# Optimization experiments

Measured on AMD Instinct MI355X. Metric: run time of the kernel, lower is better.

## Reference

```python
import jax, jax.numpy as jnp
import numpy as np

EMB = 1024
NHEAD = 16
HEAD_DIM = EMB // NHEAD  # 64
L = 2048
NEG = -1e30


def setup_inputs() -> dict:
    key = jax.random.key(0)
    ks = jax.random.split(key, 8)
    # xavier_uniform bound for square [EMB, EMB] matrices
    bound = float(np.sqrt(6.0 / (EMB + EMB)))
    def xavier(k):
        return jax.random.uniform(k, (EMB, EMB), jnp.float32, -bound, bound)
    return {
        "q": jax.random.normal(ks[0], (L, EMB), jnp.float32),
        "k": jax.random.normal(ks[1], (L, EMB), jnp.float32),
        "v": jax.random.normal(ks[2], (L, EMB), jnp.float32),
        "mask": jax.random.randint(ks[3], (NHEAD, L, L), 0, 2) > 0,
        "Wq": xavier(ks[4]),
        "Wk": xavier(ks[5]),
        "Wv": xavier(ks[6]),
        "Wo": xavier(ks[7]),
    }


def reference(q, k, v, mask, Wq, Wk, Wv, Wo):
    scaling = HEAD_DIM ** -0.5
    # F.linear(x, W) = x @ W.T ; reshape to [H, L, D]
    Q = (q @ Wq.T).reshape(L, NHEAD, HEAD_DIM).swapaxes(0, 1)
    K = (k @ Wk.T).reshape(L, NHEAD, HEAD_DIM).swapaxes(0, 1)
    V = (v @ Wv.T).reshape(L, NHEAD, HEAD_DIM).swapaxes(0, 1)
    scores = jnp.einsum("hld,hmd->hlm", Q, K) * scaling  # [H, L, L]
    scores = jnp.where(mask, jnp.asarray(NEG, scores.dtype), scores)
    p = jax.nn.softmax(scores, axis=-1)
    # attn_mask=True: multiplicative re-mask after softmax (custom path)
    p = p * (~mask).astype(p.dtype)
    # dropout is a no-op in eval mode
    attn_out = jnp.einsum("hlm,hmd->hld", p, V)  # [H, L, D]
    attn_out = attn_out.swapaxes(0, 1).reshape(L, EMB)
    return attn_out @ Wo.T
```

## Files before the change

### kernel.cpp

```cpp
#include <hip/hip_runtime.h>
#include <stdint.h>

#define EMB   1024
#define NHEAD 16
#define HDIM  64
#define SEQ   2048

typedef unsigned short ushort_t;
typedef unsigned int   uint32;
typedef __attribute__((ext_vector_type(8))) short bfrag;
typedef __attribute__((ext_vector_type(4))) float ffrag;

#define MFMA(a, b, c) __builtin_amdgcn_mfma_f32_16x16x32_bf16((a), (b), (c), 0, 0, 0)

__device__ inline ushort_t f2bf(float f) {
  uint32 u = __float_as_uint(f);
  u += 0x7FFFu + ((u >> 16) & 1u);
  return (ushort_t)(u >> 16);
}
__device__ inline uint32 pack2(float a, float b) {
  return (uint32)f2bf(a) | ((uint32)f2bf(b) << 16);
}

__device__ inline void glds16(const ushort_t* g, ushort_t* l) {
  __builtin_amdgcn_global_load_lds(
      (const __attribute__((address_space(1))) uint32*)(uintptr_t)g,
      (__attribute__((address_space(3))) uint32*)(uintptr_t)l, 16, 0, 0);
}

__global__ __launch_bounds__(256) void cvt_all(
    const float4* __restrict__ q,  const float4* __restrict__ k,  const float4* __restrict__ v,
    const float4* __restrict__ wq, const float4* __restrict__ wk, const float4* __restrict__ wv,
    const float4* __restrict__ wo,
    uint2* __restrict__ qb,  uint2* __restrict__ kb,  uint2* __restrict__ vb,
    uint2* __restrict__ wqb, uint2* __restrict__ wkb, uint2* __restrict__ wvb,
    uint2* __restrict__ wob)
{
  int t = blockIdx.x * 256 + threadIdx.x;
  int s = blockIdx.y;
  const float4* src; uint2* dst; int n4;
  switch (s) {
    case 0: src = q;  dst = qb;  n4 = (SEQ * EMB) / 4; break;
    case 1: src = k;  dst = kb;  n4 = (SEQ * EMB) / 4; break;
    case 2: src = v;  dst = vb;  n4 = (SEQ * EMB) / 4; break;
    case 3: src = wq; dst = wqb; n4 = (EMB * EMB) / 4; break;
    case 4: src = wk; dst = wkb; n4 = (EMB * EMB) / 4; break;
    case 5: src = wv; dst = wvb; n4 = (EMB * EMB) / 4; break;
    default: src = wo; dst = wob; n4 = (EMB * EMB) / 4; break;
  }
  if (t >= n4) return;
  float4 f = src[t];
  uint2 o; o.x = pack2(f.x, f.y); o.y = pack2(f.z, f.w);
  dst[t] = o;
}

template<int MODE, int BN>
__device__ inline void gemm_body(const ushort_t* A, const ushort_t* B, void* Cp,
                                 int m0, int n0, ushort_t* As, ushort_t* Bs) {
  const int tid = threadIdx.x, lane = tid & 63, w = tid >> 6;
  const int wm = (w >> 1) * 64, wn = (w & 1) * (BN / 2);
  const int col = lane & 15, g = lane >> 4;
  constexpr int TN = BN / 32;
  constexpr int BIT = BN / 32;
  constexpr int ASZ = 128 * 64;
  constexpr int BSZ = BN * 64;

  ffrag acc[4][TN] = {};

  auto stage = [&](int kt, int buf) {
    const int k0 = kt * 64;
    ushort_t* Ad = As + buf * ASZ;
    ushort_t* Bd = Bs + buf * BSZ;
    #pragma unroll
    for (int it = 0; it < 4; ++it) {
      int p = it * 256 + tid;
      int row = p >> 3, pc = p & 7;
      glds16(A + (size_t)(m0 + row) * EMB + k0 + (pc ^ (row & 7)) * 8, &Ad[p * 8]);
    }
    #pragma unroll
    for (int it = 0; it < BIT; ++it) {
      int p = it * 256 + tid;
      int row = p >> 3, pc = p & 7;
      glds16(B + (size_t)(n0 + row) * EMB + k0 + (pc ^ (row & 7)) * 8, &Bd[p * 8]);
    }
  };

  stage(0, 0);

  for (int kt = 0; kt < 16; ++kt) {
    const int buf = kt & 1;
    __syncthreads();
    if (kt < 15) stage(kt + 1, buf ^ 1);

    const ushort_t* Ac = As + buf * ASZ;
    const ushort_t* Bc = Bs + buf * BSZ;

    #pragma unroll
    for (int c = 0; c < 2; ++c) {
      bfrag av[4], bv[TN];
      #pragma unroll
      for (int t = 0; t < 4; ++t) {
        int ra = wm + t * 16 + col;
        av[t] = *(const bfrag*)&Ac[ra * 64 + ((c * 4 + g) ^ (ra & 7)) * 8];
      }
      #pragma unroll
      for (int t = 0; t < TN; ++t) {
        int rb = wn + t * 16 + col;
        bv[t] = *(const bfrag*)&Bc[rb * 64 + ((c * 4 + g) ^ (rb & 7)) * 8];
      }
      #pragma unroll
      for (int tm = 0; tm < 4; ++tm)
        #pragma unroll
        for (int tn = 0; tn < TN; ++tn)
          acc[tm][tn] = MFMA(av[tm], bv[tn], acc[tm][tn]);
    }
  }

  const int rbase = g * 4;
  #pragma unroll
  for (int tm = 0; tm < 4; ++tm)
    #pragma unroll
    for (int tn = 0; tn < TN; ++tn)
      #pragma unroll
      for (int r = 0; r < 4; ++r) {
        int m = m0 + wm + tm * 16 + rbase + r;
        int n = n0 + wn + tn * 16 + col;
        float vv = acc[tm][tn][r];
        if (MODE == 0) {
          ((ushort_t*)Cp)[((size_t)(n >> 6) * SEQ + m) * HDIM + (n & 63)] = f2bf(vv);
        } else if (MODE == 1) {
          ((ushort_t*)Cp)[((size_t)(m >> 6) * HDIM + (m & 63)) * SEQ + n] = f2bf(vv);
        } else {
          ((float*)Cp)[(size_t)m * EMB + n] = vv;
        }
      }
}

__global__ __launch_bounds__(256) void gemm_qkv(
    const ushort_t* __restrict__ qb, const ushort_t* __restrict__ kb, const ushort_t* __restrict__ vb,
    const ushort_t* __restrict__ Wqb, const ushort_t* __restrict__ Wkb, const ushort_t* __restrict__ Wvb,
    ushort_t* __restrict__ Qb, ushort_t* __restrict__ Kb, ushort_t* __restrict__ Vtb)
{
  __shared__ ushort_t As[2 * 128 * 64];
  __shared__ ushort_t Bs[2 * 64 * 64];
  const int z = blockIdx.y, bid = blockIdx.x;
  if (z == 0) {
    gemm_body<0, 64>(qb, Wqb, Qb, (bid >> 4) * 128, (bid & 15) * 64, As, Bs);
  } else if (z == 1) {
    gemm_body<0, 64>(kb, Wkb, Kb, (bid >> 4) * 128, (bid & 15) * 64, As, Bs);
  } else {
    gemm_body<1, 64>(Wvb, vb, Vtb, (bid >> 5) * 128, (bid & 31) * 64, As, Bs);
  }
}

__global__ __launch_bounds__(256) void gemm_out(
    const ushort_t* __restrict__ A, const ushort_t* __restrict__ B, float* __restrict__ C)
{
  __shared__ ushort_t As[2 * 128 * 64];
  __shared__ ushort_t Bs[2 * 64 * 64];
  gemm_body<2, 64>(A, B, (void*)C, blockIdx.y * 128, blockIdx.x * 64, As, Bs);
}

__global__ __launch_bounds__(256) void attn_mfma(
    const ushort_t* __restrict__ Qb,
    const ushort_t* __restrict__ Kb,
    const ushort_t* __restrict__ Vtb,
    const void*    __restrict__ maskp,
    ushort_t* __restrict__ attnb)
{
  __shared__ ushort_t Ks[2][64 * 64];
  __shared__ ushort_t Vs[2][64 * 64];
  __shared__ ushort_t Ps[4][16 * 72];

  const int tid  = threadIdx.x;
  const int lane = tid & 63;
  const int w    = tid >> 6;
  const int h    = blockIdx.y;
  const int l0   = blockIdx.x * 64;
  const int col  = lane & 15, g = lane >> 4, kg8 = g * 8, rbase = g * 4;

  uint32 mw0 = ((const uint32*)maskp)[lane];
  bool is4 = (mw0 == 0u) || (mw0 == 1u) || (mw0 == 0x3F800000u);
  const bool flag4 = (__ballot(!is4) == 0ull);

  ushort_t* pw = &Ps[w][0];

  {
    int rl = lane >> 2, seg = (lane & 3) * 16;
    const uint4* pq = (const uint4*)(Qb + ((size_t)h * SEQ + l0 + w * 16 + rl) * HDIM + seg);
    uint4 q0 = pq[0], q1 = pq[1];
    *(uint4*)&pw[rl * 72 + seg] = q0;
    *(uint4*)&pw[rl * 72 + seg + 8] = q1;
  }
  bfrag qf[2];
  qf[0] = *(const bfrag*)&pw[col * 72 + kg8];
  qf[1] = *(const bfrag*)&pw[col * 72 + 32 + kg8];

  auto stage = [&](int t2, int b) {
    const int cb = t2 * 64;
    #pragma unroll
    for (int it = 0; it < 2; ++it) {
      int p = it * 256 + tid;
      int row = p >> 3, pc = p & 7;
      int sc = (pc ^ (row & 7)) * 8;
      glds16(Kb  + ((size_t)h * SEQ + cb + row) * HDIM + sc, &Ks[b][p * 8]);
      glds16(Vtb + ((size_t)h * HDIM + row) * SEQ + cb + sc, &Vs[b][p * 8]);
    }
  };

  const size_t mrow = (size_t)h * SEQ + l0 + w * 16 + col;
  uint4 mn[4], mc[4];
  auto load_mask = [&](int t2) {
    const int cb = t2 * 64 + rbase;
    if (flag4) {
      const uint32* m32 = (const uint32*)maskp + mrow * SEQ + cb;
      #pragma unroll
      for (int tn = 0; tn < 4; ++tn) mn[tn] = *(const uint4*)(m32 + tn * 16);
    } else {
      const unsigned char* m8 = (const unsigned char*)maskp + mrow * SEQ + cb;
      #pragma unroll
      for (int tn = 0; tn < 4; ++tn) {
        uint32 b4 = *(const uint32*)(m8 + tn * 16);
        mn[tn].x = b4 & 0xFFu; mn[tn].y = (b4 >> 8) & 0xFFu;
        mn[tn].z = (b4 >> 16) & 0xFFu; mn[tn].w = b4 >> 24;
      }
    }
  };

  stage(0, 0);
  load_mask(0);
  __syncthreads();

  float lsum = 0.f;
  ffrag oacc[4] = {};

  for (int t = 0; t < 32; ++t) {
    const int buf = t & 1;

    #pragma unroll
    for (int tn = 0; tn < 4; ++tn) mc[tn] = mn[tn];
    if (t < 31) {
      stage(t + 1, buf ^ 1);
      load_mask(t + 1);
    }

    ffrag s[4] = {};
    #pragma unroll
    for (int c = 0; c < 2; ++c)
      #pragma unroll
      for (int tn = 0; tn < 4; ++tn) {
        int row = tn * 16 + col;
        bfrag kf = *(const bfrag*)&Ks[buf][row * 64 + ((c * 4 + g) ^ (row & 7)) * 8];
        s[tn] = MFMA(kf, qf[c], s[tn]);
      }

    #pragma unroll
    for (int tn = 0; tn < 4; ++tn) {
      float p0 = mc[tn].x ? 0.f : __expf(s[tn][0] * 0.125f);
      float p1 = mc[tn].y ? 0.f : __expf(s[tn][1] * 0.125f);
      float p2 = mc[tn].z ? 0.f : __expf(s[tn][2] * 0.125f);
      float p3 = mc[tn].w ? 0.f : __expf(s[tn][3] * 0.125f);
      lsum += (p0 + p1) + (p2 + p3);
      uint2 pk; pk.x = pack2(p0, p1); pk.y = pack2(p2, p3);
      *(uint2*)&pw[col * 72 + tn * 16 + rbase] = pk;
    }

    #pragma unroll
    for (int c = 0; c < 2; ++c) {
      bfrag af = *(const bfrag*)&pw[col * 72 + c * 32 + kg8];
      #pragma unroll
      for (int tn = 0; tn < 4; ++tn) {
        int row = tn * 16 + col;
        bfrag vf = *(const bfrag*)&Vs[buf][row * 64 + ((c * 4 + g) ^ (row & 7)) * 8];
        oacc[tn] = MFMA(af, vf, oacc[tn]);
      }
    }

    __syncthreads();
  }

  float s_ = lsum;
  s_ += __shfl_xor(s_, 16, 64);
  s_ += __shfl_xor(s_, 32, 64);
  float invf = (s_ > 0.f) ? (1.0f / s_) : 0.0f;
  float inv[4];
  #pragma unroll
  for (int r = 0; r < 4; ++r) inv[r] = __shfl(invf, rbase + r, 64);

  #pragma unroll
  for (int tn = 0; tn < 4; ++tn)
    #pragma unroll
    for (int r = 0; r < 4; ++r) {
      int qg = l0 + w * 16 + rbase + r;
      attnb[(size_t)qg * EMB + h * HDIM + tn * 16 + col] = f2bf(oacc[tn][r] * inv[r]);
    }
}

extern "C" void kernel_launch(void* const* d_in, const int* in_sizes, int n_in,
                              void* d_out, int out_size, void* d_ws, size_t ws_size,
                              hipStream_t stream) {
  const float* q    = (const float*)d_in[0];
  const float* k    = (const float*)d_in[1];
  const float* v    = (const float*)d_in[2];
  const void*  mask =               d_in[3];
  const float* Wq   = (const float*)d_in[4];
  const float* Wk   = (const float*)d_in[5];
  const float* Wv   = (const float*)d_in[6];
  const float* Wo   = (const float*)d_in[7];

  char* ws = (char*)d_ws;
  const size_t MB = 1024 * 1024;
  ushort_t* qb    = (ushort_t*)(ws);
  ushort_t* kb    = (ushort_t*)(ws + 4  * MB);
  ushort_t* vb    = (ushort_t*)(ws + 8  * MB);
  ushort_t* Wqb   = (ushort_t*)(ws + 12 * MB);
  ushort_t* Wkb   = (ushort_t*)(ws + 14 * MB);
  ushort_t* Wvb   = (ushort_t*)(ws + 16 * MB);
  ushort_t* Wob   = (ushort_t*)(ws + 18 * MB);
  ushort_t* Qb    = (ushort_t*)(ws + 20 * MB);
  ushort_t* Kb    = (ushort_t*)(ws + 24 * MB);
  ushort_t* Vtb   = (ushort_t*)(ws + 28 * MB);
  ushort_t* attnb = qb;

  cvt_all<<<dim3((SEQ * EMB / 4 + 255) / 256, 7), 256, 0, stream>>>(
      (const float4*)q, (const float4*)k, (const float4*)v,
      (const float4*)Wq, (const float4*)Wk, (const float4*)Wv, (const float4*)Wo,
      (uint2*)qb, (uint2*)kb, (uint2*)vb,
      (uint2*)Wqb, (uint2*)Wkb, (uint2*)Wvb, (uint2*)Wob);

  gemm_qkv<<<dim3(256, 3), 256, 0, stream>>>(qb, kb, vb, Wqb, Wkb, Wvb, Qb, Kb, Vtb);

  attn_mfma<<<dim3(SEQ / 64, NHEAD), 256, 0, stream>>>(Qb, Kb, Vtb, mask, attnb);

  gemm_out<<<dim3(16, 16), 256, 0, stream>>>(attnb, Wob, (float*)d_out);
}
```

Measured before the change: 447.2 us.

## Reorder block tile mapping, XOR-swizzle P buffer, use exp2 in softmax

Remaps block indices in the QKV and output GEMMs so consecutive blocks walk the M dimension first, and flattens the attention grid so the 16 heads for one query tile run next to each other. The intent is better L2 and MALL reuse of shared weight and mask data. It also replaces the padded P/Q scratch stride with an XOR swizzle to avoid LDS bank conflicts, and switches exp to exp2 with a prefolded log2e scale. These are several independent tweaks, and their effects on cache locality and LDS conflicts may partly cancel.

```diff
diff --git a/kernel.cpp b/kernel.cpp
--- a/kernel.cpp
+++ b/kernel.cpp
@@ -145,11 +145,11 @@
   __shared__ ushort_t Bs[2 * 64 * 64];
   const int z = blockIdx.y, bid = blockIdx.x;
   if (z == 0) {
-    gemm_body<0, 64>(qb, Wqb, Qb, (bid >> 4) * 128, (bid & 15) * 64, As, Bs);
+    gemm_body<0, 64>(qb, Wqb, Qb, (bid & 15) * 128, (bid >> 4) * 64, As, Bs);
   } else if (z == 1) {
-    gemm_body<0, 64>(kb, Wkb, Kb, (bid >> 4) * 128, (bid & 15) * 64, As, Bs);
+    gemm_body<0, 64>(kb, Wkb, Kb, (bid & 15) * 128, (bid >> 4) * 64, As, Bs);
   } else {
-    gemm_body<1, 64>(Wvb, vb, Vtb, (bid >> 5) * 128, (bid & 31) * 64, As, Bs);
+    gemm_body<1, 64>(Wvb, vb, Vtb, (bid & 7) * 128, (bid >> 3) * 64, As, Bs);
   }
 }
 
@@ -158,7 +158,7 @@
 {
   __shared__ ushort_t As[2 * 128 * 64];
   __shared__ ushort_t Bs[2 * 64 * 64];
-  gemm_body<2, 64>(A, B, (void*)C, blockIdx.y * 128, blockIdx.x * 64, As, Bs);
+  gemm_body<2, 64>(A, B, (void*)C, blockIdx.x * 128, blockIdx.y * 64, As, Bs);
 }
 
 __global__ __launch_bounds__(256) void attn_mfma(
@@ -170,31 +170,32 @@
 {
   __shared__ ushort_t Ks[2][64 * 64];
   __shared__ ushort_t Vs[2][64 * 64];
-  __shared__ ushort_t Ps[4][16 * 72];
+  __shared__ ushort_t Ps[4 * 16 * 64];
 
   const int tid  = threadIdx.x;
   const int lane = tid & 63;
   const int w    = tid >> 6;
-  const int h    = blockIdx.y;
-  const int l0   = blockIdx.x * 64;
+  const int h    = blockIdx.x & 15;
+  const int l0   = (blockIdx.x >> 4) * 64;
   const int col  = lane & 15, g = lane >> 4, kg8 = g * 8, rbase = g * 4;
 
   uint32 mw0 = ((const uint32*)maskp)[lane];
   bool is4 = (mw0 == 0u) || (mw0 == 1u) || (mw0 == 0x3F800000u);
   const bool flag4 = (__ballot(!is4) == 0ull);
 
-  ushort_t* pw = &Ps[w][0];
+  ushort_t* pw = &Ps[w * 16 * 64];
+  auto pidx = [&](int row, int k) { return row * 64 + (k ^ ((row & 7) * 8)); };
 
   {
     int rl = lane >> 2, seg = (lane & 3) * 16;
     const uint4* pq = (const uint4*)(Qb + ((size_t)h * SEQ + l0 + w * 16 + rl) * HDIM + seg);
     uint4 q0 = pq[0], q1 = pq[1];
-    *(uint4*)&pw[rl * 72 + seg] = q0;
-    *(uint4*)&pw[rl * 72 + seg + 8] = q1;
+    *(uint4*)&pw[pidx(rl, seg)] = q0;
+    *(uint4*)&pw[pidx(rl, seg + 8)] = q1;
   }
   bfrag qf[2];
-  qf[0] = *(const bfrag*)&pw[col * 72 + kg8];
-  qf[1] = *(const bfrag*)&pw[col * 72 + 32 + kg8];
+  qf[0] = *(const bfrag*)&pw[pidx(col, kg8)];
+  qf[1] = *(const bfrag*)&pw[pidx(col, 32 + kg8)];
 
   auto stage = [&](int t2, int b) {
     const int cb = t2 * 64;
@@ -231,6 +232,8 @@
   load_mask(0);
   __syncthreads();
 
+  const float SCL = 0.125f * 1.44269504089f;
+
   float lsum = 0.f;
   ffrag oacc[4] = {};
 
@@ -256,18 +259,18 @@
 
     #pragma unroll
     for (int tn = 0; tn < 4; ++tn) {
-      float p0 = mc[tn].x ? 0.f : __expf(s[tn][0] * 0.125f);
-      float p1 = mc[tn].y ? 0.f : __expf(s[tn][1] * 0.125f);
-      float p2 = mc[tn].z ? 0.f : __expf(s[tn][2] * 0.125f);
-      float p3 = mc[tn].w ? 0.f : __expf(s[tn][3] * 0.125f);
+      float p0 = mc[tn].x ? 0.f : exp2f(s[tn][0] * SCL);
+      float p1 = mc[tn].y ? 0.f : exp2f(s[tn][1] * SCL);
+      float p2 = mc[tn].z ? 0.f : exp2f(s[tn][2] * SCL);
+      float p3 = mc[tn].w ? 0.f : exp2f(s[tn][3] * SCL);
       lsum += (p0 + p1) + (p2 + p3);
       uint2 pk; pk.x = pack2(p0, p1); pk.y = pack2(p2, p3);
-      *(uint2*)&pw[col * 72 + tn * 16 + rbase] = pk;
+      *(uint2*)&pw[pidx(col, tn * 16 + rbase)] = pk;
     }
 
     #pragma unroll
     for (int c = 0; c < 2; ++c) {
-      bfrag af = *(const bfrag*)&pw[col * 72 + c * 32 + kg8];
+      bfrag af = *(const bfrag*)&pw[pidx(col, c * 32 + kg8)];
       #pragma unroll
       for (int tn = 0; tn < 4; ++tn) {
         int row = tn * 16 + col;
@@ -330,7 +333,7 @@
 
   gemm_qkv<<<dim3(256, 3), 256, 0, stream>>>(qb, kb, vb, Wqb, Wkb, Wvb, Qb, Kb, Vtb);
 
-  attn_mfma<<<dim3(SEQ / 64, NHEAD), 256, 0, stream>>>(Qb, Kb, Vtb, mask, attnb);
+  attn_mfma<<<dim3(512), 256, 0, stream>>>(Qb, Kb, Vtb, mask, attnb);
 
   gemm_out<<<dim3(16, 16), 256, 0, stream>>>(attnb, Wob, (float*)d_out);
 }
```

After: 450.2 us. No clear change (+0.7%).
